# Kernel optimization log

Hardware: AMD Instinct MI355X
Metric: run time of the kernel (lower is better)

## Reference

```python
import jax, jax.numpy as jnp
import numpy as np

# Dimensions inferred from VSSBlockOneWay(hidden_dim=256, ssm_d_state=64, forward_type='m0_noz')
B_, L_, D_ = 8, 2048, 256      # batch, seq_len, d_model
DIN, N_, P_ = 512, 64, 64      # d_inner = 2*d_model, d_state, head_dim
H_ = DIN // P_                 # n_heads = 8


def _ln(x, w, b, eps=1e-5):
    m = x.mean(-1, keepdims=True)
    v = ((x - m) ** 2).mean(-1, keepdims=True)
    return (x - m) * jax.lax.rsqrt(v + eps) * w + b


def setup_inputs() -> dict:
    key = jax.random.key(0)
    ks = jax.random.split(key, 8)
    s = lambda k, shape, sc: jax.random.normal(k, shape, jnp.float32) * sc
    return dict(
        src=jax.random.normal(ks[0], (B_, L_, D_), jnp.float32),
        ln_w=jnp.ones((D_,), jnp.float32), ln_b=jnp.zeros((D_,), jnp.float32),
        W_in=s(ks[1], (D_, DIN), 0.02),
        conv_w=s(ks[2], (DIN, 1, 3), 0.1),            # depthwise conv1d kernel
        conv_b=jnp.zeros((DIN,), jnp.float32),
        W_xproj=s(ks[3], (DIN, H_ + 2 * N_), 0.02),   # -> (dt | B | C)
        dt_bias=s(ks[4], (H_,), 0.1),
        A_log=jnp.log(jnp.arange(1, H_ + 1, dtype=jnp.float32)),  # Mamba2 A-init
        Ds=jnp.ones((H_,), jnp.float32),
        oln_w=jnp.ones((DIN,), jnp.float32), oln_b=jnp.zeros((DIN,), jnp.float32),
        W_out=s(ks[5], (DIN, D_), 0.02),
    )


def reference(src, ln_w, ln_b, W_in, conv_w, conv_b, W_xproj, dt_bias,
              A_log, Ds, oln_w, oln_b, W_out):
    B, L, D = src.shape
    H, N, P = H_, N_, P_
    x = _ln(src, ln_w, ln_b)
    u = x @ W_in                                                    # (B,L,DIN)
    # depthwise conv over sequence, SAME padding (VMamba uses non-causal dwconv)
    uc = jax.lax.conv_general_dilated(
        u.transpose(0, 2, 1), conv_w, (1,), 'SAME',
        feature_group_count=DIN, dimension_numbers=('NCH', 'OIH', 'NCH'))
    u = jax.nn.gelu((uc + conv_b[None, :, None]).transpose(0, 2, 1),
                    approximate=False)                              # (B,L,DIN)
    dbc = u @ W_xproj                                               # (B,L,H+2N)
    dt = jax.nn.softplus(dbc[..., :H] + dt_bias)                    # (B,L,H)
    Bm = dbc[..., H:H + N]                                          # (B,L,N)
    Cm = dbc[..., H + N:]                                           # (B,L,N)
    A = -jnp.exp(A_log)                                             # (H,)
    decay = jnp.exp(dt * A)                                         # (B,L,H)
    xh = u.reshape(B, L, H, P)
    dtx = dt[..., None] * xh                                        # (B,L,H,P)

    def step(h, inp):
        dec_t, dtx_t, B_t, C_t = inp
        # h: (B,H,P,N)
        h = h * dec_t[:, :, None, None] + dtx_t[..., None] * B_t[:, None, None, :]
        y = jnp.einsum('bhpn,bn->bhp', h, C_t)
        return h, y

    h0 = jnp.zeros((B, H, P, N), u.dtype)
    inputs = (decay.transpose(1, 0, 2), dtx.transpose(1, 0, 2, 3),
              Bm.transpose(1, 0, 2), Cm.transpose(1, 0, 2))
    _, ys = jax.lax.scan(step, h0, inputs)                          # (L,B,H,P)
    y = ys.transpose(1, 0, 2, 3) + xh * Ds[None, None, :, None]
    y = _ln(y.reshape(B, L, DIN), oln_w, oln_b)
    # dropout / drop_path are identity at inference
    return src + y @ W_out
```

## Files before the change

### kernel.cpp

```cpp
#include <hip/hip_runtime.h>
#include <hip/hip_bf16.h>
#include <cmath>

typedef __hip_bfloat16 bf16;
typedef short bf16x8 __attribute__((ext_vector_type(8)));
typedef short bf16x4v __attribute__((ext_vector_type(4)));
typedef float f32x4 __attribute__((ext_vector_type(4)));

constexpr int B_ = 8, L_ = 2048, D_ = 256, DIN_ = 512;
constexpr int H_ = 8, N_ = 64, P_ = 64;
constexpr int BL_ = B_ * L_;
constexpr int NCH_ = 136;
constexpr int Q_ = 64;
constexpr int NC_ = L_ / Q_;

static __device__ __forceinline__ float b2f(bf16 x) { return __bfloat162float(x); }
static __device__ __forceinline__ bf16  f2b(float x) { return __float2bfloat16(x); }
static __device__ __forceinline__ bf16  rawb(short s) { __hip_bfloat16_raw r; r.x = (unsigned short)s; return (bf16)r; }
static __device__ __forceinline__ float sane(float v) { return (fabsf(v) <= 1e30f) ? v : 0.f; }
static __device__ __forceinline__ float loadx(const void* p, size_t i, bool isbf) {
    return isbf ? b2f(((const bf16*)p)[i]) : ((const float*)p)[i];
}
static __device__ __forceinline__ bf16x8 load8x(const void* p, size_t off, bool isbf) {
    if (isbf) return *(const bf16x8*)((const bf16*)p + off);
    const float4* fp = (const float4*)((const float*)p + off);
    float4 f0 = fp[0], f1 = fp[1];
    bf16 t[8] = {f2b(f0.x), f2b(f0.y), f2b(f0.z), f2b(f0.w),
                 f2b(f1.x), f2b(f1.y), f2b(f1.z), f2b(f1.w)};
    return *(bf16x8*)t;
}
static __device__ __forceinline__ int swz(int row, int col) { return col ^ (((row >> 3) & 7) * 8); }

static __device__ __forceinline__ f32x4 mfma16(bf16x8 a, bf16x8 b, f32x4 c) {
    return __builtin_amdgcn_mfma_f32_16x16x32_bf16(a, b, c, 0, 0, 0);
}
#define ONES8 bf16x8{16256, 16256, 16256, 16256, 16256, 16256, 16256, 16256}

__global__ __launch_bounds__(256) void prep_k(const void* __restrict__ Win, const void* __restrict__ Wx,
                       const void* __restrict__ Wo,
                       const void* __restrict__ ln_w, const void* __restrict__ ln_b,
                       const void* __restrict__ oln_w, const void* __restrict__ oln_b,
                       bf16* __restrict__ WinT, bf16* __restrict__ WxT, bf16* __restrict__ WoT,
                       float* __restrict__ colsum1, float* __restrict__ bias1,
                       float* __restrict__ colsum2, float* __restrict__ bias2,
                       const unsigned short* __restrict__ flagp) {
    const bool isbf = flagp[0] != 0;
    const int bx = blockIdx.x, tid = threadIdx.x;
    if (bx < 88) {
        __shared__ float T[64][65];
        if (bx < 32) {
            int d0 = (bx & 3) * 64, n0 = (bx >> 2) * 64;
#pragma unroll
            for (int i = 0; i < 16; i++) {
                int e = tid + 256 * i; int r = e >> 6, c = e & 63;
                T[r][c] = loadx(Win, (size_t)(d0 + r) * DIN_ + n0 + c, isbf);
            }
            __syncthreads();
#pragma unroll
            for (int i = 0; i < 16; i++) {
                int e = tid + 256 * i; int r = e >> 6, c = e & 63;
                WinT[(size_t)(n0 + r) * D_ + d0 + c] = f2b(loadx(ln_w, d0 + c, isbf) * T[c][r]);
            }
        } else if (bx < 64) {
            int t2 = bx - 32;
            int k0 = (t2 & 7) * 64, d0 = (t2 >> 3) * 64;
#pragma unroll
            for (int i = 0; i < 16; i++) {
                int e = tid + 256 * i; int r = e >> 6, c = e & 63;
                T[r][c] = loadx(Wo, (size_t)(k0 + r) * D_ + d0 + c, isbf);
            }
            __syncthreads();
#pragma unroll
            for (int i = 0; i < 16; i++) {
                int e = tid + 256 * i; int r = e >> 6, c = e & 63;
                WoT[(size_t)(d0 + r) * DIN_ + k0 + c] = f2b(loadx(oln_w, k0 + c, isbf) * T[c][r]);
            }
        } else {
            int t3 = bx - 64;
            int i0 = (t3 & 7) * 64, j0 = (t3 >> 3) * 64;
#pragma unroll
            for (int i = 0; i < 16; i++) {
                int e = tid + 256 * i; int r = e >> 6, c = e & 63;
                int j = j0 + c;
                T[r][c] = (j < NCH_) ? loadx(Wx, (size_t)(i0 + r) * NCH_ + j, isbf) : 0.f;
            }
            __syncthreads();
#pragma unroll
            for (int i = 0; i < 16; i++) {
                int e = tid + 256 * i; int r = e >> 6, c = e & 63;
                WxT[(size_t)(j0 + r) * DIN_ + i0 + c] = f2b(T[c][r]);
            }
        }
        return;
    }
    const int o = (bx - 88) * 4 + (tid >> 6);
    const int lane = tid & 63;
    float cs = 0.f, bs = 0.f;
    if (o < DIN_) {
        int n = o;
        for (int i = lane; i < D_; i += 64) {
            float wv = loadx(Win, (size_t)i * DIN_ + n, isbf);
            cs += loadx(ln_w, i, isbf) * wv;
            bs += loadx(ln_b, i, isbf) * wv;
        }
    } else {
        int d = o - DIN_;
        for (int k = lane; k < DIN_; k += 64) {
            float wv = loadx(Wo, (size_t)k * D_ + d, isbf);
            cs += loadx(oln_w, k, isbf) * wv;
            bs += loadx(oln_b, k, isbf) * wv;
        }
    }
#pragma unroll
    for (int off = 32; off >= 1; off >>= 1) { cs += __shfl_xor(cs, off); bs += __shfl_xor(bs, off); }
    if (lane == 0) {
        if (o < DIN_) { colsum1[o] = cs; bias1[o] = bs; }
        else          { colsum2[o - DIN_] = cs; bias2[o - DIN_] = bs; }
    }
}

__global__ __launch_bounds__(256) void gemm1conv_k(const void* __restrict__ src,
                                                   const bf16* __restrict__ WinT,
                                                   const float* __restrict__ colsum1,
                                                   const float* __restrict__ bias1,
                                                   const void* __restrict__ cw,
                                                   const void* __restrict__ cb,
                                                   bf16* __restrict__ u,
                                                   const unsigned short* __restrict__ flagp) {
    const bool isbf = flagp[0] != 0;
    constexpr int K = D_;
    constexpr int STR = K + 8;
    constexpr int CH = K / 8;
    __shared__ bf16 Blds[64 * STR];
    __shared__ bf16 U[130][72];
    const int tid = threadIdx.x;
    const int n0 = blockIdx.y * 64;
    const int m0 = blockIdx.x * 128;
    const int l0i = m0 & (L_ - 1);
#pragma unroll
    for (int i = 0; i < 64 * CH / 256; i++) {
        int e = tid + 256 * i;
        int r = e / CH, cch = e % CH;
        bf16x8 v = *(const bf16x8*)(WinT + (size_t)(n0 + r) * K + cch * 8);
        *(bf16x8*)(&Blds[r * STR + cch * 8]) = v;
    }
    __syncthreads();
    const int wave = tid >> 6, lane = tid & 63;
    const int quad = lane >> 4, l16 = lane & 15;
    const int mw = m0 + wave * 32;
    const bf16x8 ones = ONES8;
    f32x4 acc[2][4], accS[2], accS2[2];
#pragma unroll
    for (int i = 0; i < 2; i++) {
        accS[i] = f32x4{0.f, 0.f, 0.f, 0.f};
        accS2[i] = f32x4{0.f, 0.f, 0.f, 0.f};
#pragma unroll
        for (int j = 0; j < 4; j++) acc[i][j] = f32x4{0.f, 0.f, 0.f, 0.f};
    }
    const size_t r0 = (size_t)(mw + l16) * K + quad * 8;
    const size_t r1 = r0 + (size_t)16 * K;
#pragma unroll
    for (int k0 = 0; k0 < K; k0 += 32) {
        bf16x8 a0 = load8x(src, r0 + k0, isbf);
        bf16x8 a1 = load8x(src, r1 + k0, isbf);
        accS[0]  = mfma16(a0, ones, accS[0]);
        accS2[0] = mfma16(a0, a0, accS2[0]);
        accS[1]  = mfma16(a1, ones, accS[1]);
        accS2[1] = mfma16(a1, a1, accS2[1]);
#pragma unroll
        for (int i = 0; i < 4; i++) {
            bf16x8 bb = *(const bf16x8*)(&Blds[(16 * i + l16) * STR + k0 + quad * 8]);
            acc[0][i] = mfma16(a0, bb, acc[0][i]);
            acc[1][i] = mfma16(a1, bb, acc[1][i]);
        }
    }
    float cs[4], bsv[4];
#pragma unroll
    for (int i = 0; i < 4; i++) { int n = n0 + 16 * i + l16; cs[i] = colsum1[n]; bsv[i] = bias1[n]; }
#pragma unroll
    for (int rb = 0; rb < 2; rb++)
#pragma unroll
        for (int r = 0; r < 4; r++) {
            int rl = quad * 4 + r;
            float sv  = accS[rb][r];
            float s2v = __shfl(accS2[rb][r], (quad << 4) + rl);
            float mean = sv * (1.f / D_);
            float var  = s2v * (1.f / D_) - mean * mean;
            float rs = rsqrtf(fmaxf(var, 0.f) + 1e-5f);
            int rloc = wave * 32 + rb * 16 + rl;
#pragma unroll
            for (int i = 0; i < 4; i++) {
                float v = rs * (acc[rb][i][r] - mean * cs[i]) + bsv[i];
                U[1 + rloc][16 * i + l16] = f2b(v);
            }
        }
    if (tid < 128) {
        const int hrow = tid >> 6;
        const int n = tid & 63;
        const int urow = hrow ? 129 : 0;
        const bool valid = hrow ? (l0i != L_ - 128) : (l0i != 0);
        float val = 0.f;
        if (valid) {
            const int g = hrow ? (m0 + 128) : (m0 - 1);
            const bf16* brow = &Blds[n * STR];
            float dot = 0.f, s = 0.f, s2 = 0.f;
            for (int k8 = 0; k8 < CH; k8++) {
                bf16x8 bb = *(const bf16x8*)(brow + k8 * 8);
#pragma unroll
                for (int t = 0; t < 8; t++) {
                    float a = b2f(f2b(loadx(src, (size_t)g * K + k8 * 8 + t, isbf)));
                    dot += a * b2f(rawb(bb[t]));
                    s += a; s2 += a * a;
                }
            }
            float mean = s * (1.f / D_);
            float var  = s2 * (1.f / D_) - mean * mean;
            float rs = rsqrtf(fmaxf(var, 0.f) + 1e-5f);
            val = rs * (dot - mean * colsum1[n0 + n]) + bias1[n0 + n];
        }
        U[urow][n] = f2b(val);
    }
    __syncthreads();
    const int cg = tid & 7, rg = tid >> 3;
    const int c8 = cg * 8;
    float w0[8], w1[8], w2[8], bia[8];
#pragma unroll
    for (int t = 0; t < 8; t++) {
        int chn = n0 + c8 + t;
        w0[t]  = loadx(cw, chn * 3 + 0, isbf);
        w1[t]  = loadx(cw, chn * 3 + 1, isbf);
        w2[t]  = loadx(cw, chn * 3 + 2, isbf);
        bia[t] = loadx(cb, chn, isbf);
    }
#pragma unroll
    for (int i = 0; i < 4; i++) {
        int r = rg * 4 + i;
        bf16x8 vl = *(const bf16x8*)(&U[r][c8]);
        bf16x8 vm = *(const bf16x8*)(&U[r + 1][c8]);
        bf16x8 vr = *(const bf16x8*)(&U[r + 2][c8]);
        bf16 ob[8];
#pragma unroll
        for (int t = 0; t < 8; t++) {
            float a = bia[t] + w1[t] * b2f(rawb(vm[t]))
                    + w0[t] * b2f(rawb(vl[t])) + w2[t] * b2f(rawb(vr[t]));
            float ge = 0.5f * a * (1.f + erff(a * 0.70710678118f));
            ob[t] = f2b(ge);
        }
        *(bf16x8*)(u + (size_t)(m0 + r) * DIN_ + n0 + c8) = *(bf16x8*)ob;
    }
}

template<int MODE>
__global__ __launch_bounds__(256) void gemmB_k(const bf16* __restrict__ A,
                                               const bf16* __restrict__ BT,
                                               void* __restrict__ Cout,
                                               const void* __restrict__ resid,
                                               const float* __restrict__ colsum,
                                               const float* __restrict__ biasv,
                                               const void* __restrict__ dt_bias,
                                               const void* __restrict__ A_log,
                                               float* __restrict__ dtg,
                                               float* __restrict__ dtAg,
                                               const unsigned short* __restrict__ flagp) {
    const bool isbf = flagp[0] != 0;
    constexpr int K = 512;
    constexpr int KH = 256;
    constexpr int STR = KH + 8;
    constexpr int CH = KH / 8;
    __shared__ bf16 Blds[64 * STR];
    const int tid = threadIdx.x;
    const int n0 = blockIdx.y * 64;
    const int wave = tid >> 6, lane = tid & 63;
    const int quad = lane >> 4, l16 = lane & 15;
    const int m0 = blockIdx.x * 128 + wave * 32;
    const bf16x8 ones = ONES8;
    f32x4 acc[2][4], accS[2], accS2[2];
#pragma unroll
    for (int i = 0; i < 2; i++) {
        accS[i] = f32x4{0.f, 0.f, 0.f, 0.f};
        accS2[i] = f32x4{0.f, 0.f, 0.f, 0.f};
#pragma unroll
        for (int j = 0; j < 4; j++) acc[i][j] = f32x4{0.f, 0.f, 0.f, 0.f};
    }
    const bf16* a0p = A + (size_t)(m0 + l16) * K + quad * 8;
    const bf16* a1p = a0p + (size_t)16 * K;
#pragma unroll
    for (int kh = 0; kh < 2; kh++) {
        if (kh) __syncthreads();
#pragma unroll
        for (int i = 0; i < 64 * CH / 256; i++) {
            int e = tid + 256 * i;
            int r = e / CH, cch = e % CH;
            bf16x8 v = *(const bf16x8*)(BT + (size_t)(n0 + r) * K + kh * KH + cch * 8);
            *(bf16x8*)(&Blds[r * STR + cch * 8]) = v;
        }
        __syncthreads();
        const bf16* ah0 = a0p + kh * KH;
        const bf16* ah1 = a1p + kh * KH;
#pragma unroll 4
        for (int k0 = 0; k0 < KH; k0 += 32) {
            bf16x8 a0 = *(const bf16x8*)(ah0 + k0);
            bf16x8 a1 = *(const bf16x8*)(ah1 + k0);
            if (MODE == 1) {
                accS[0]  = mfma16(a0, ones, accS[0]);
                accS2[0] = mfma16(a0, a0, accS2[0]);
                accS[1]  = mfma16(a1, ones, accS[1]);
                accS2[1] = mfma16(a1, a1, accS2[1]);
            }
#pragma unroll
            for (int i = 0; i < 4; i++) {
                bf16x8 bb = *(const bf16x8*)(&Blds[(16 * i + l16) * STR + k0 + quad * 8]);
                acc[0][i] = mfma16(a0, bb, acc[0][i]);
                acc[1][i] = mfma16(a1, bb, acc[1][i]);
            }
        }
    }
    if (MODE == 0) {
#pragma unroll
        for (int rb = 0; rb < 2; rb++)
#pragma unroll
            for (int r = 0; r < 4; r++) {
                int m = m0 + rb * 16 + quad * 4 + r;
#pragma unroll
                for (int i = 0; i < 4; i++) {
                    int n = n0 + 16 * i + l16;
                    if (n < NCH_) ((bf16*)Cout)[(size_t)m * NCH_ + n] = f2b(acc[rb][i][r]);
                }
            }
        if (blockIdx.y == 0 && l16 < 8) {
            float bb = loadx(dt_bias, l16, isbf);
            float Ah = -__expf(fminf(loadx(A_log, l16, isbf), 30.f));
#pragma unroll
            for (int rb = 0; rb < 2; rb++)
#pragma unroll
                for (int r = 0; r < 4; r++) {
                    int m = m0 + rb * 16 + quad * 4 + r;
                    float raw = acc[rb][0][r] + bb;
                    float sp = raw > 20.f ? raw : log1pf(__expf(raw));
                    sp = fminf(sp, 60.f);
                    dtg[(size_t)m * H_ + l16]  = sp;
                    dtAg[(size_t)m * H_ + l16] = sp * Ah;
                }
        }
    } else {
        float cs[4], bsv[4];
#pragma unroll
        for (int i = 0; i < 4; i++) { int n = n0 + 16 * i + l16; cs[i] = colsum[n]; bsv[i] = biasv[n]; }
#pragma unroll
        for (int rb = 0; rb < 2; rb++)
#pragma unroll
            for (int r = 0; r < 4; r++) {
                int rl = quad * 4 + r;
                float sv  = accS[rb][r];
                float s2v = __shfl(accS2[rb][r], (quad << 4) + rl);
                float mean = sv * (1.f / K);
                float var  = s2v * (1.f / K) - mean * mean;
                float rs = rsqrtf(fmaxf(var, 0.f) + 1e-5f);
                int m = m0 + rb * 16 + rl;
#pragma unroll
                for (int i = 0; i < 4; i++) {
                    int n = n0 + 16 * i + l16;
                    size_t o = (size_t)m * D_ + n;
                    float v = rs * (acc[rb][i][r] - mean * cs[i]) + bsv[i] + loadx(resid, o, isbf);
                    v = sane(v);
                    if (isbf) ((bf16*)Cout)[o] = f2b(v);
                    else      ((float*)Cout)[o] = v;
                }
            }
    }
}

__global__ __launch_bounds__(256) void chunk_state_k(const bf16* __restrict__ ubuf,
                                                     const bf16* __restrict__ dbcb,
                                                     const float* __restrict__ dtg,
                                                     const float* __restrict__ dtAg,
                                                     bf16* __restrict__ HS,
                                                     float* __restrict__ cdg) {
    const int idx = blockIdx.x;
    const int c = idx & 31, h = (idx >> 5) & 7, b = idx >> 8;
    const int bh = b * 8 + h;
    const int blbase = b * L_ + c * Q_;
    __shared__ bf16 Xw[64][72];
    __shared__ bf16 BTb[64][72];
    __shared__ float fj[64];
    const int tid = threadIdx.x;
    if (tid < 64) {
        int j = tid;
        float dA  = dtAg[(size_t)(blbase + j) * H_ + h];
        float dtv = dtg[(size_t)(blbase + j) * H_ + h];
        float v = dA;
#pragma unroll
        for (int off = 1; off < 64; off <<= 1) { float t = __shfl_up(v, off); if (j >= off) v += t; }
        float segEnd = __shfl(v, 63);
        fj[j] = __expf(fminf(segEnd - v, 0.f)) * dtv;
        if (j == 0) cdg[bh * NC_ + c] = __expf(fminf(segEnd, 0.f));
    }
    __syncthreads();
    {
        const int jr = tid >> 3, p8 = (tid & 7) * 8;
#pragma unroll
        for (int it = 0; it < 2; it++) {
            int j = jr + 32 * it;
            float fs = fj[j];
            bf16x8 xv = *(const bf16x8*)(ubuf + (size_t)(blbase + j) * DIN_ + h * 64 + p8);
            bf16x8 bv = *(const bf16x8*)(dbcb + (size_t)(blbase + j) * NCH_ + 8 + p8);
#pragma unroll
            for (int t = 0; t < 8; t++) {
                int p = p8 + t;
                Xw[p][swz(p, j)]  = f2b(fs * b2f(rawb(xv[t])));
                BTb[p][swz(p, j)] = rawb(bv[t]);
            }
        }
    }
    __syncthreads();
    const int wave = tid >> 6, lane = tid & 63, quad = lane >> 4, l16 = lane & 15;
    const int p0 = wave * 16;
    f32x4 acc[4];
#pragma unroll
    for (int i = 0; i < 4; i++) acc[i] = f32x4{0.f, 0.f, 0.f, 0.f};
#pragma unroll
    for (int ks = 0; ks < 2; ks++) {
        int pa = p0 + l16;
        bf16x8 a = *(const bf16x8*)(&Xw[pa][swz(pa, ks * 32 + quad * 8)]);
#pragma unroll
        for (int nt = 0; nt < 4; nt++) {
            int nb = nt * 16 + l16;
            bf16x8 bb = *(const bf16x8*)(&BTb[nb][swz(nb, ks * 32 + quad * 8)]);
            acc[nt] = mfma16(a, bb, acc[nt]);
        }
    }
    size_t slot = (size_t)(bh * NC_ + c) * 4096;
#pragma unroll
    for (int nt = 0; nt < 4; nt++)
#pragma unroll
        for (int r = 0; r < 4; r++) {
            int p = p0 + quad * 4 + r, n = nt * 16 + l16;
            HS[slot + p * 64 + n] = f2b(sane(acc[nt][r]));
        }
}

__global__ __launch_bounds__(256) void chunk_rec_k(bf16* __restrict__ HS,
                                                   const float* __restrict__ cdg) {
    const int bh = blockIdx.x >> 2, sub = blockIdx.x & 3;
    const int eo = sub * 1024 + threadIdx.x * 4;
    bf16* base = HS + (size_t)bh * (NC_ * 4096) + eo;
    bf16x4v v[NC_];
#pragma unroll
    for (int c = 0; c < NC_; c++) v[c] = *(const bf16x4v*)(base + (size_t)c * 4096);
    float cdr[NC_];
#pragma unroll
    for (int c = 0; c < NC_; c++) cdr[c] = cdg[bh * NC_ + c];
    float h0 = 0.f, h1 = 0.f, h2 = 0.f, h3 = 0.f;
#pragma unroll
    for (int c = 0; c < NC_; c++) {
        bf16 ob[4] = {f2b(h0), f2b(h1), f2b(h2), f2b(h3)};
        *(bf16x4v*)(base + (size_t)c * 4096) = *(bf16x4v*)ob;
        float cd = cdr[c];
        h0 = cd * h0 + b2f(rawb(v[c][0]));
        h1 = cd * h1 + b2f(rawb(v[c][1]));
        h2 = cd * h2 + b2f(rawb(v[c][2]));
        h3 = cd * h3 + b2f(rawb(v[c][3]));
    }
}

__global__ __launch_bounds__(256) void chunk_out_k(bf16* __restrict__ ubuf,
                                                   const bf16* __restrict__ dbcb,
                                                   const float* __restrict__ dtg,
                                                   const float* __restrict__ dtAg,
                                                   const bf16* __restrict__ HS,
                                                   const void* __restrict__ Ds,
                                                   bf16* __restrict__ ybuf,
                                                   const unsigned short* __restrict__ flagp) {
    const bool isbf = flagp[0] != 0;
    const int idx = blockIdx.x;
    const int c = idx & 31, h = (idx >> 5) & 7, b = idx >> 8;
    const int bh = b * 8 + h;
    const int blbase = b * L_ + c * Q_;
    const size_t slotbase = (size_t)(bh * NC_ + c) * 4096;
    __shared__ bf16 Xb[64][72];
    __shared__ bf16 Gb[64][72];
    __shared__ float segL[64], PL[64], dtL[64];
    const int tid = threadIdx.x;
    if (tid < 64) {
        int j = tid;
        float dA  = dtAg[(size_t)(blbase + j) * H_ + h];
        float dtv = dtg[(size_t)(blbase + j) * H_ + h];
        float v = dA;
#pragma unroll
        for (int off = 1; off < 64; off <<= 1) { float t = __shfl_up(v, off); if (j >= off) v += t; }
        segL[j] = v;
        PL[j]   = __expf(fminf(v, 0.f));
        dtL[j]  = dtv;
    }
    {
        const int rr = tid >> 3, k8 = (tid & 7) * 8;
#pragma unroll
        for (int it = 0; it < 2; it++) {
            int r = rr + 32 * it;
            bf16x8 xv = *(const bf16x8*)(ubuf + (size_t)(blbase + r) * DIN_ + h * 64 + k8);
#pragma unroll
            for (int t = 0; t < 8; t++) { int p = k8 + t; Xb[p][swz(p, r)] = rawb(xv[t]); }
        }
    }
    __syncthreads();
    const int wave = tid >> 6, lane = tid & 63, quad = lane >> 4, l16 = lane & 15;
    const int l0 = wave * 16;
    f32x4 g[4];
#pragma unroll
    for (int i = 0; i < 4; i++) g[i] = f32x4{0.f, 0.f, 0.f, 0.f};
#pragma unroll
    for (int ks = 0; ks < 2; ks++) {
        bf16x8 a = *(const bf16x8*)(dbcb + (size_t)(blbase + l0 + l16) * NCH_ + 72 + ks * 32 + quad * 8);
#pragma unroll
        for (int jt = 0; jt < 4; jt++) {
            bf16x8 bb = *(const bf16x8*)(dbcb + (size_t)(blbase + jt * 16 + l16) * NCH_ + 8 + ks * 32 + quad * 8);
            g[jt] = mfma16(a, bb, g[jt]);
        }
    }
#pragma unroll
    for (int jt = 0; jt < 4; jt++) {
        int j = jt * 16 + l16;
#pragma unroll
        for (int r = 0; r < 4; r++) {
            int l = l0 + quad * 4 + r;
            float e = __expf(fminf(segL[l] - segL[j], 0.f));
            float gv = (j <= l) ? sane(g[jt][r]) * e * dtL[j] : 0.f;
            Gb[l][swz(l, j)] = f2b(sane(gv));
        }
    }
    __syncthreads();
    f32x4 y1[4], y2[4];
#pragma unroll
    for (int i = 0; i < 4; i++) { y1[i] = f32x4{0.f, 0.f, 0.f, 0.f}; y2[i] = f32x4{0.f, 0.f, 0.f, 0.f}; }
#pragma unroll
    for (int ks = 0; ks < 2; ks++) {
        int la = l0 + l16;
        bf16x8 ag = *(const bf16x8*)(&Gb[la][swz(la, ks * 32 + quad * 8)]);
        bf16x8 ac = *(const bf16x8*)(dbcb + (size_t)(blbase + la) * NCH_ + 72 + ks * 32 + quad * 8);
#pragma unroll
        for (int pt = 0; pt < 4; pt++) {
            int pb = pt * 16 + l16;
            bf16x8 bx = *(const bf16x8*)(&Xb[pb][swz(pb, ks * 32 + quad * 8)]);
            bf16x8 bhf = *(const bf16x8*)(HS + slotbase + (size_t)pb * 64 + ks * 32 + quad * 8);
            y1[pt] = mfma16(ag, bx, y1[pt]);
            y2[pt] = mfma16(ac, bhf, y2[pt]);
        }
    }
    float dsH = loadx(Ds, h, isbf);
#pragma unroll
    for (int pt = 0; pt < 4; pt++) {
        int p = pt * 16 + l16;
#pragma unroll
        for (int r = 0; r < 4; r++) {
            int l = l0 + quad * 4 + r;
            float yv = y1[pt][r] + PL[l] * y2[pt][r] + dsH * b2f(Xb[p][swz(p, l)]);
            ybuf[(size_t)(blbase + l) * DIN_ + h * 64 + p] = f2b(sane(yv));
        }
    }
}

extern "C" void kernel_launch(void* const* d_in, const int* in_sizes, int n_in,
                              void* d_out, int out_size, void* d_ws, size_t ws_size,
                              hipStream_t stream) {
    const void* src     = d_in[0];
    const void* ln_w    = d_in[1];
    const void* ln_b    = d_in[2];
    const void* W_in    = d_in[3];
    const void* conv_w  = d_in[4];
    const void* conv_b  = d_in[5];
    const void* W_xproj = d_in[6];
    const void* dt_bias = d_in[7];
    const void* A_log   = d_in[8];
    const void* Ds      = d_in[9];
    const void* oln_w   = d_in[10];
    const void* oln_b   = d_in[11];
    const void* W_out   = d_in[12];
    const unsigned short* flagp = (const unsigned short*)ln_w;

    char* w = (char*)d_ws;
    size_t off = 0;
    auto alloc = [&](size_t bytes) { void* p = w + off; off += (bytes + 255) & ~(size_t)255; return p; };
    char*   regB   = (char*)alloc((size_t)BL_ * DIN_ * 2);
    char*   regC   = (char*)alloc((size_t)BL_ * DIN_ * 2);
    bf16*   dbcb   = (bf16*)alloc((size_t)BL_ * NCH_ * 2);
    float*  dtg    = (float*)alloc((size_t)BL_ * H_ * 4);
    float*  dtAg   = (float*)alloc((size_t)BL_ * H_ * 4);
    bf16*   WinT   = (bf16*)alloc((size_t)DIN_ * D_ * 2);
    bf16*   WxT    = (bf16*)alloc((size_t)192 * DIN_ * 2);
    bf16*   WoT    = (bf16*)alloc((size_t)D_ * DIN_ * 2);
    float*  colsum1= (float*)alloc(DIN_ * 4);
    float*  bias1  = (float*)alloc(DIN_ * 4);
    float*  colsum2= (float*)alloc(D_ * 4);
    float*  bias2  = (float*)alloc(D_ * 4);
    float*  cdg    = (float*)alloc((size_t)64 * NC_ * 4);

    bf16* HS    = (bf16*)regB;
    bf16* ubuf  = (bf16*)regC;
    bf16* ybuf  = (bf16*)regC;

    prep_k<<<88 + 192, 256, 0, stream>>>(W_in, W_xproj, W_out, ln_w, ln_b, oln_w, oln_b,
                                         WinT, WxT, WoT, colsum1, bias1, colsum2, bias2, flagp);
    gemm1conv_k<<<dim3(BL_ / 128, 8), 256, 0, stream>>>(src, WinT, colsum1, bias1,
                                                        conv_w, conv_b, ubuf, flagp);
    gemmB_k<0><<<dim3(BL_ / 128, 3), 256, 0, stream>>>(ubuf, WxT, dbcb, nullptr, nullptr, nullptr,
                                                       dt_bias, A_log, dtg, dtAg, flagp);
    chunk_state_k<<<B_ * H_ * NC_, 256, 0, stream>>>(ubuf, dbcb, dtg, dtAg, HS, cdg);
    chunk_rec_k<<<256, 256, 0, stream>>>(HS, cdg);
    chunk_out_k<<<B_ * H_ * NC_, 256, 0, stream>>>(ubuf, dbcb, dtg, dtAg, HS, Ds, ybuf, flagp);
    gemmB_k<1><<<dim3(BL_ / 128, 4), 256, 0, stream>>>(ybuf, WoT, d_out, src, colsum2, bias2,
                                                       nullptr, nullptr, nullptr, nullptr, flagp);
}
```

Before: 242.1 us.

## Use MFMA for conv halo rows and drop LDS/sync in chunk kernels

The halo-row projection in the fused LN+in-proj+conv kernel is now computed with MFMA across all four waves instead of a scalar per-thread dot product over K run by 128 threads. In chunk_state_k and chunk_out_k, every wave now computes the per-lane cumulative decay scan redundantly and shares values through wave shuffles instead of shared arrays. This removes one __syncthreads in chunk_state_k and issues the global loads before the scan to overlap latency. The cost is redundant scan work per wave and extra shuffle instructions.

Measured after the change: 210.9 us. 12.9% less time.

```diff
diff --git a/kernel.cpp b/kernel.cpp
--- a/kernel.cpp
+++ b/kernel.cpp
@@ -194,31 +194,51 @@
                 U[1 + rloc][16 * i + l16] = f2b(v);
             }
         }
-    if (tid < 128) {
-        const int hrow = tid >> 6;
-        const int n = tid & 63;
-        const int urow = hrow ? 129 : 0;
-        const bool valid = hrow ? (l0i != L_ - 128) : (l0i != 0);
-        float val = 0.f;
+    {
+        const int hseg = wave >> 1;
+        const int chal = wave & 1;
+        const bool valid = hseg ? (l0i != L_ - 128) : (l0i != 0);
+        const int urow = hseg ? 129 : 0;
+        const int rsel = hseg ? 0 : 3;
+        const int qsel = hseg ? 0 : 3;
+        const int lsel = hseg ? 0 : 63;
         if (valid) {
-            const int g = hrow ? (m0 + 128) : (m0 - 1);
-            const bf16* brow = &Blds[n * STR];
-            float dot = 0.f, s = 0.f, s2 = 0.f;
-            for (int k8 = 0; k8 < CH; k8++) {
-                bf16x8 bb = *(const bf16x8*)(brow + k8 * 8);
-#pragma unroll
-                for (int t = 0; t < 8; t++) {
-                    float a = b2f(f2b(loadx(src, (size_t)g * K + k8 * 8 + t, isbf)));
-                    dot += a * b2f(rawb(bb[t]));
-                    s += a; s2 += a * a;
+            const int gm0 = hseg ? (m0 + 128) : (m0 - 16);
+            f32x4 ha[2], hS, hS2;
+            ha[0] = f32x4{0.f, 0.f, 0.f, 0.f}; ha[1] = f32x4{0.f, 0.f, 0.f, 0.f};
+            hS = f32x4{0.f, 0.f, 0.f, 0.f};   hS2 = f32x4{0.f, 0.f, 0.f, 0.f};
+            const size_t hr = (size_t)(gm0 + l16) * K + quad * 8;
+#pragma unroll
+            for (int k0 = 0; k0 < K; k0 += 32) {
+                bf16x8 a = load8x(src, hr + k0, isbf);
+                hS  = mfma16(a, ones, hS);
+                hS2 = mfma16(a, a, hS2);
+#pragma unroll
+                for (int i = 0; i < 2; i++) {
+                    bf16x8 bb = *(const bf16x8*)(&Blds[(32 * chal + 16 * i + l16) * STR + k0 + quad * 8]);
+                    ha[i] = mfma16(a, bb, ha[i]);
                 }
             }
-            float mean = s * (1.f / D_);
-            float var  = s2 * (1.f / D_) - mean * mean;
+            float sv  = __shfl(hS[rsel],  lsel);
+            float s2v = __shfl(hS2[rsel], lsel);
+            float mean = sv * (1.f / D_);
+            float var  = s2v * (1.f / D_) - mean * mean;
             float rs = rsqrtf(fmaxf(var, 0.f) + 1e-5f);
-            val = rs * (dot - mean * colsum1[n0 + n]) + bias1[n0 + n];
-        }
-        U[urow][n] = f2b(val);
+            if (quad == qsel) {
+#pragma unroll
+                for (int i = 0; i < 2; i++) {
+                    int n = n0 + 32 * chal + 16 * i + l16;
+                    float v = rs * (ha[i][rsel] - mean * colsum1[n]) + bias1[n];
+                    U[urow][32 * chal + 16 * i + l16] = f2b(v);
+                }
+            }
+        } else {
+            if (quad == qsel) {
+#pragma unroll
+                for (int i = 0; i < 2; i++)
+                    U[urow][32 * chal + 16 * i + l16] = f2b(0.f);
+            }
+        }
     }
     __syncthreads();
     const int cg = tid & 7, rg = tid >> 3;
@@ -382,38 +402,33 @@
     const int blbase = b * L_ + c * Q_;
     __shared__ bf16 Xw[64][72];
     __shared__ bf16 BTb[64][72];
-    __shared__ float fj[64];
     const int tid = threadIdx.x;
-    if (tid < 64) {
-        int j = tid;
-        float dA  = dtAg[(size_t)(blbase + j) * H_ + h];
-        float dtv = dtg[(size_t)(blbase + j) * H_ + h];
-        float v = dA;
-#pragma unroll
-        for (int off = 1; off < 64; off <<= 1) { float t = __shfl_up(v, off); if (j >= off) v += t; }
-        float segEnd = __shfl(v, 63);
-        fj[j] = __expf(fminf(segEnd - v, 0.f)) * dtv;
-        if (j == 0) cdg[bh * NC_ + c] = __expf(fminf(segEnd, 0.f));
+    const int lane = tid & 63;
+    float dA  = dtAg[(size_t)(blbase + lane) * H_ + h];
+    float dtv = dtg[(size_t)(blbase + lane) * H_ + h];
+    const int jr = tid >> 3, p8 = (tid & 7) * 8;
+    bf16x8 xv0 = *(const bf16x8*)(ubuf + (size_t)(blbase + jr) * DIN_ + h * 64 + p8);
+    bf16x8 bv0 = *(const bf16x8*)(dbcb + (size_t)(blbase + jr) * NCH_ + 8 + p8);
+    bf16x8 xv1 = *(const bf16x8*)(ubuf + (size_t)(blbase + jr + 32) * DIN_ + h * 64 + p8);
+    bf16x8 bv1 = *(const bf16x8*)(dbcb + (size_t)(blbase + jr + 32) * NCH_ + 8 + p8);
+    float v = dA;
+#pragma unroll
+    for (int off = 1; off < 64; off <<= 1) { float t = __shfl_up(v, off); if (lane >= off) v += t; }
+    float segEnd = __shfl(v, 63);
+    float fjl = __expf(fminf(segEnd - v, 0.f)) * dtv;
+    if (tid == 0) cdg[bh * NC_ + c] = __expf(fminf(segEnd, 0.f));
+    float fs0 = __shfl(fjl, jr);
+    float fs1 = __shfl(fjl, jr + 32);
+#pragma unroll
+    for (int t = 0; t < 8; t++) {
+        int p = p8 + t;
+        Xw[p][swz(p, jr)]       = f2b(fs0 * b2f(rawb(xv0[t])));
+        BTb[p][swz(p, jr)]      = rawb(bv0[t]);
+        Xw[p][swz(p, jr + 32)]  = f2b(fs1 * b2f(rawb(xv1[t])));
+        BTb[p][swz(p, jr + 32)] = rawb(bv1[t]);
     }
     __syncthreads();
-    {
-        const int jr = tid >> 3, p8 = (tid & 7) * 8;
-#pragma unroll
-        for (int it = 0; it < 2; it++) {
-            int j = jr + 32 * it;
-            float fs = fj[j];
-            bf16x8 xv = *(const bf16x8*)(ubuf + (size_t)(blbase + j) * DIN_ + h * 64 + p8);
-            bf16x8 bv = *(const bf16x8*)(dbcb + (size_t)(blbase + j) * NCH_ + 8 + p8);
-#pragma unroll
-            for (int t = 0; t < 8; t++) {
-                int p = p8 + t;
-                Xw[p][swz(p, j)]  = f2b(fs * b2f(rawb(xv[t])));
-                BTb[p][swz(p, j)] = rawb(bv[t]);
-            }
-        }
-    }
-    __syncthreads();
-    const int wave = tid >> 6, lane = tid & 63, quad = lane >> 4, l16 = lane & 15;
+    const int wave = tid >> 6, quad = lane >> 4, l16 = lane & 15;
     const int p0 = wave * 16;
     f32x4 acc[4];
 #pragma unroll
@@ -479,31 +494,25 @@
     const size_t slotbase = (size_t)(bh * NC_ + c) * 4096;
     __shared__ bf16 Xb[64][72];
     __shared__ bf16 Gb[64][72];
-    __shared__ float segL[64], PL[64], dtL[64];
     const int tid = threadIdx.x;
-    if (tid < 64) {
-        int j = tid;
-        float dA  = dtAg[(size_t)(blbase + j) * H_ + h];
-        float dtv = dtg[(size_t)(blbase + j) * H_ + h];
-        float v = dA;
-#pragma unroll
-        for (int off = 1; off < 64; off <<= 1) { float t = __shfl_up(v, off); if (j >= off) v += t; }
-        segL[j] = v;
-        PL[j]   = __expf(fminf(v, 0.f));
-        dtL[j]  = dtv;
-    }
-    {
-        const int rr = tid >> 3, k8 = (tid & 7) * 8;
-#pragma unroll
-        for (int it = 0; it < 2; it++) {
-            int r = rr + 32 * it;
-            bf16x8 xv = *(const bf16x8*)(ubuf + (size_t)(blbase + r) * DIN_ + h * 64 + k8);
-#pragma unroll
-            for (int t = 0; t < 8; t++) { int p = k8 + t; Xb[p][swz(p, r)] = rawb(xv[t]); }
-        }
+    const int lane = tid & 63;
+    float dA  = dtAg[(size_t)(blbase + lane) * H_ + h];
+    float dtl = dtg[(size_t)(blbase + lane) * H_ + h];
+    const int rr = tid >> 3, k8 = (tid & 7) * 8;
+    bf16x8 xva = *(const bf16x8*)(ubuf + (size_t)(blbase + rr) * DIN_ + h * 64 + k8);
+    bf16x8 xvb = *(const bf16x8*)(ubuf + (size_t)(blbase + rr + 32) * DIN_ + h * 64 + k8);
+    float segl = dA;
+#pragma unroll
+    for (int off = 1; off < 64; off <<= 1) { float t = __shfl_up(segl, off); if (lane >= off) segl += t; }
+    float PLl = __expf(fminf(segl, 0.f));
+#pragma unroll
+    for (int t = 0; t < 8; t++) {
+        int p = k8 + t;
+        Xb[p][swz(p, rr)]      = rawb(xva[t]);
+        Xb[p][swz(p, rr + 32)] = rawb(xvb[t]);
     }
     __syncthreads();
-    const int wave = tid >> 6, lane = tid & 63, quad = lane >> 4, l16 = lane & 15;
+    const int wave = tid >> 6, quad = lane >> 4, l16 = lane & 15;
     const int l0 = wave * 16;
     f32x4 g[4];
 #pragma unroll
@@ -520,11 +529,13 @@
 #pragma unroll
     for (int jt = 0; jt < 4; jt++) {
         int j = jt * 16 + l16;
+        float segj = __shfl(segl, j);
+        float dtj  = __shfl(dtl, j);
 #pragma unroll
         for (int r = 0; r < 4; r++) {
             int l = l0 + quad * 4 + r;
-            float e = __expf(fminf(segL[l] - segL[j], 0.f));
-            float gv = (j <= l) ? sane(g[jt][r]) * e * dtL[j] : 0.f;
+            float e = __expf(fminf(__shfl(segl, l) - segj, 0.f));
+            float gv = (j <= l) ? sane(g[jt][r]) * e * dtj : 0.f;
             Gb[l][swz(l, j)] = f2b(sane(gv));
         }
     }
@@ -553,7 +564,7 @@
 #pragma unroll
         for (int r = 0; r < 4; r++) {
             int l = l0 + quad * 4 + r;
-            float yv = y1[pt][r] + PL[l] * y2[pt][r] + dsH * b2f(Xb[p][swz(p, l)]);
+            float yv = y1[pt][r] + __shfl(PLl, l) * y2[pt][r] + dsH * b2f(Xb[p][swz(p, l)]);
             ybuf[(size_t)(blbase + l) * DIN_ + h * 64 + p] = f2b(sane(yv));
         }
     }
```
